# Performance work log

Hardware: AMD Instinct MI355X
Metric: run time of the kernel (lower is better)

The kernel has to match this reference:

```python
import jax, jax.numpy as jnp
import numpy as np

B, T, D, H = 32, 8192, 128, 128

def setup_inputs() -> dict:
    key = jax.random.key(0)
    k1, k2, k3, k4, k5 = jax.random.split(key, 5)
    return {
        "encoder_outputs": jax.random.normal(k1, (B, T, D), dtype=jnp.float32),
        "decoder_hidden": jax.random.normal(k2, (B, H), dtype=jnp.float32),
        "W1": jax.random.normal(k3, (D, D), dtype=jnp.float32) * 0.08,
        "W2": jax.random.normal(k4, (H, D), dtype=jnp.float32) * 0.08,
        "V": jax.random.normal(k5, (D, 1), dtype=jnp.float32) * 0.08,
    }

def reference(encoder_outputs, decoder_hidden, W1, W2, V):
    # score: [B, T, D] = tanh(enc @ W1 + (dec @ W2)[:, None, :])
    score = jnp.tanh(jnp.einsum('btd,de->bte', encoder_outputs, W1)
                     + jnp.einsum('bh,hd->bd', decoder_hidden, W2)[:, None, :])
    # logits: [B, T, 1]; softmax over time axis (axis=1)
    logits = jnp.einsum('btd,do->bto', score, V)
    attention_weights = jax.nn.softmax(logits, axis=1)
    # context: [B, D] weighted sum over T
    context_vector = jnp.sum(attention_weights * encoder_outputs, axis=1)
    return context_vector, attention_weights
```

## Files before the change

### kernel.cpp

```cpp
#include <hip/hip_runtime.h>

#define B_ 32
#define T_ 8192
#define D_ 128
#define MBLK 128
#define NCHUNK 64

typedef __attribute__((ext_vector_type(8))) _Float16 half8;
typedef __attribute__((ext_vector_type(4))) _Float16 half4;
typedef __attribute__((ext_vector_type(4))) float floatx4;

__device__ __forceinline__ float tanh_fast(float x) {
    float e = __expf(2.0f * x);
    return 1.0f - __fdividef(2.0f, e + 1.0f);
}

__global__ void prep_kernel(const float* __restrict__ W1, half8* __restrict__ W1frag,
                            const float* __restrict__ dec, const float* __restrict__ W2,
                            float* __restrict__ bias) {
    int bid = blockIdx.x, tid = threadIdx.x;
    if (bid < 8) {
        int tg = bid * 256 + tid;
        int kk = tg >> 9, ni = (tg >> 6) & 7, lane = tg & 63;
        half8 h;
        #pragma unroll
        for (int j = 0; j < 8; ++j) {
            int k = kk * 32 + ((lane >> 4) * 8) + j;
            int n = ni * 16 + (lane & 15);
            h[j] = (_Float16)W1[k * 128 + n];
        }
        W1frag[tg] = h;
    } else {
        int b = (bid - 8) * 2 + (tid >> 7);
        int d = tid & 127;
        float acc = 0.f;
        for (int h = 0; h < 128; ++h)
            acc += dec[b * 128 + h] * W2[h * 128 + d];
        bias[b * 128 + d] = acc;
    }
}

__global__ __launch_bounds__(512)
void main_kernel(const float* __restrict__ enc, const half8* __restrict__ W1frag,
                 const float* __restrict__ bias, const float* __restrict__ V,
                 float* __restrict__ out_w, float* __restrict__ s_part,
                 float* __restrict__ c_part)
{
    __shared__ __align__(16) char smem_u[32768];
    __shared__ __align__(16) float red[MBLK];
    __shared__ __align__(16) float ews[MBLK];
    __shared__ __align__(16) float c_red[8][128];
    __shared__ float sp[2];

    half8* bfr = (half8*)smem_u;
    char*  encl = smem_u;

    const int tid = threadIdx.x;
    const int l = tid & 63;
    const int w = tid >> 6;
    const int g = l >> 4;
    const int bid = blockIdx.x;
    const int b = bid >> 6;
    const int chunk = bid & 63;
    const int arow = w * 16 + (l & 15);
    const float* rowp = enc + ((long)b * T_ + (long)chunk * MBLK + arow) * D_ + g * 8;

    #pragma unroll
    for (int q = 0; q < 4; ++q)
        __builtin_amdgcn_global_load_lds(
            (const __attribute__((address_space(1))) void*)(W1frag + q * 512 + tid),
            (__attribute__((address_space(3))) void*)(bfr + q * 512 + (w << 6)),
            16, 0, 0);

    half8 afr[4];
    #pragma unroll
    for (int kk = 0; kk < 4; ++kk) {
        float4 f0 = *(const float4*)(rowp + kk * 32);
        float4 f1 = *(const float4*)(rowp + kk * 32 + 4);
        half8 a;
        a[0] = (_Float16)f0.x; a[1] = (_Float16)f0.y;
        a[2] = (_Float16)f0.z; a[3] = (_Float16)f0.w;
        a[4] = (_Float16)f1.x; a[5] = (_Float16)f1.y;
        a[6] = (_Float16)f1.z; a[7] = (_Float16)f1.w;
        afr[kk] = a;
    }

    float bs[8], vv[8];
    #pragma unroll
    for (int ni = 0; ni < 8; ++ni) {
        int n = ni * 16 + (l & 15);
        bs[ni] = bias[b * 128 + n];
        vv[ni] = V[n];
    }
    __syncthreads();

    floatx4 acc[8];
    #pragma unroll
    for (int ni = 0; ni < 8; ++ni) acc[ni] = (floatx4)0.0f;

    #pragma unroll
    for (int kk = 0; kk < 4; ++kk)
        #pragma unroll
        for (int ni = 0; ni < 8; ++ni)
            acc[ni] = __builtin_amdgcn_mfma_f32_16x16x32_f16(
                          afr[kk], bfr[(kk * 8 + ni) * 64 + l], acc[ni], 0, 0, 0);

    __syncthreads();

    {
        const int asw = (arow & 7) << 4;
        #pragma unroll
        for (int kk = 0; kk < 4; ++kk) {
            int byte = arow * 256 + (((kk * 64) + (g * 16)) ^ asw);
            *(half8*)(encl + byte) = afr[kk];
        }
    }

    float p[4];
    #pragma unroll
    for (int j2 = 0; j2 < 4; ++j2) {
        float q = 0.f;
        #pragma unroll
        for (int ni = 0; ni < 8; ++ni)
            q += tanh_fast(acc[ni][j2] + bs[ni]) * vv[ni];
        #pragma unroll
        for (int mk = 1; mk < 16; mk <<= 1)
            q += __shfl_xor(q, mk);
        p[j2] = q;
    }
    if ((l & 15) == 0) {
        floatx4 v4 = {p[0], p[1], p[2], p[3]};
        *(floatx4*)(&red[w * 16 + g * 4]) = v4;
        *(floatx4*)(out_w + (long)b * T_ + chunk * MBLK + w * 16 + g * 4) = v4;
    }
    __syncthreads();

    if (tid < 128) {
        float ew = __expf(red[tid]);
        ews[tid] = ew;
        float s = ew;
        #pragma unroll
        for (int mk = 1; mk < 64; mk <<= 1) s += __shfl_xor(s, mk);
        if ((tid & 63) == 0) sp[tid >> 6] = s;
    }
    __syncthreads();
    if (tid == 0) s_part[b * NCHUNK + chunk] = sp[0] + sp[1];

    if (tid < 256) {
        const int rg = tid >> 5, dg = tid & 31;
        floatx4 cc = (floatx4)0.0f;
        #pragma unroll
        for (int rr = 0; rr < 16; ++rr) {
            int r = rg * 16 + rr;
            float wgt = ews[r];
            half4 h = *(const half4*)(encl + (r * 256 + ((dg * 8) ^ ((r & 7) << 4))));
            #pragma unroll
            for (int i = 0; i < 4; ++i) cc[i] += wgt * (float)h[i];
        }
        *(floatx4*)(&c_red[rg][dg * 4]) = cc;
    }
    __syncthreads();
    if (tid < 128) {
        float s = 0.f;
        #pragma unroll
        for (int gg = 0; gg < 8; ++gg) s += c_red[gg][tid];
        c_part[((long)b * NCHUNK + chunk) * 128 + tid] = s;
    }
}

__global__ __launch_bounds__(256)
void tail_kernel(const float* __restrict__ s_part, const float* __restrict__ c_part,
                 float* __restrict__ ctx, float* __restrict__ out_w)
{
    __shared__ float stats[1];
    __shared__ float part[2][128];
    int bid = blockIdx.x, tid = threadIdx.x;
    int b = bid >> 4, j = bid & 15;

    if (tid < 64) {
        float s = s_part[b * 64 + tid];
        #pragma unroll
        for (int mk = 1; mk < 64; mk <<= 1) s += __shfl_xor(s, mk);
        if (tid == 0) stats[0] = __fdividef(1.0f, s);
    }
    __syncthreads();
    float inv = stats[0];

    if (j == 0) {
        int d = tid & 127, h = tid >> 7;
        float acc = 0.f;
        #pragma unroll 4
        for (int ch = h * 32; ch < h * 32 + 32; ++ch)
            acc += c_part[((long)b * 64 + ch) * 128 + d];
        part[h][d] = acc;
        __syncthreads();
        if (tid < 128)
            ctx[b * 128 + tid] = (part[0][tid] + part[1][tid]) * inv;
    }

    float* ow = out_w + (long)b * T_ + j * 512;
    #pragma unroll
    for (int q = 0; q < 2; ++q) {
        int i = q * 256 + tid;
        ow[i] = __expf(ow[i]) * inv;
    }
}

extern "C" void kernel_launch(void* const* d_in, const int* in_sizes, int n_in,
                              void* d_out, int out_size, void* d_ws, size_t ws_size,
                              hipStream_t stream)
{
    const float* enc = (const float*)d_in[0];
    const float* dec = (const float*)d_in[1];
    const float* W1  = (const float*)d_in[2];
    const float* W2  = (const float*)d_in[3];
    const float* V   = (const float*)d_in[4];

    float* ctx  = (float*)d_out;
    float* outw = ctx + B_ * D_;

    float* ws     = (float*)d_ws;
    float* bias   = ws;
    float* s_part = bias + 4096;
    float* c_part = s_part + 2048;
    half8* W1frag = (half8*)(c_part + (long)B_ * NCHUNK * 128);

    prep_kernel<<<24, 256, 0, stream>>>(W1, W1frag, dec, W2, bias);
    main_kernel<<<B_ * NCHUNK, 512, 0, stream>>>(enc, W1frag, bias, V, outw, s_part, c_part);
    tail_kernel<<<B_ * 16, 256, 0, stream>>>(s_part, c_part, ctx, outw);
}
```

Before: 49.61 us.

## Process two chunks per block with register prefetch of next encoder tile

Each block now handles two consecutive 128-row chunks. The W1 fragment LDS load is amortized over both chunks, and the next chunk's encoder rows are prefetched into registers while the current chunk runs its MFMA and softmax work. W1 fragments and the encoder staging buffer now get separate LDS regions instead of aliasing, which removes one barrier per chunk. The costs are more LDS per block, more live registers, and half as many blocks (1024), which may leave the GPU less full. Launch bounds now request 4 waves per EU.

```diff
diff --git a/kernel.cpp b/kernel.cpp
--- a/kernel.cpp
+++ b/kernel.cpp
@@ -5,6 +5,7 @@
 #define D_ 128
 #define MBLK 128
 #define NCHUNK 64
+#define CPB 2
 
 typedef __attribute__((ext_vector_type(8))) _Float16 half8;
 typedef __attribute__((ext_vector_type(4))) _Float16 half4;
@@ -40,50 +41,35 @@
     }
 }
 
-__global__ __launch_bounds__(512)
+__global__ __launch_bounds__(512, 4)
 void main_kernel(const float* __restrict__ enc, const half8* __restrict__ W1frag,
                  const float* __restrict__ bias, const float* __restrict__ V,
                  float* __restrict__ out_w, float* __restrict__ s_part,
                  float* __restrict__ c_part)
 {
-    __shared__ __align__(16) char smem_u[32768];
+    __shared__ __align__(16) half8 bfr[2048];
+    __shared__ __align__(16) char encl[32768];
     __shared__ __align__(16) float red[MBLK];
     __shared__ __align__(16) float ews[MBLK];
     __shared__ __align__(16) float c_red[8][128];
     __shared__ float sp[2];
-
-    half8* bfr = (half8*)smem_u;
-    char*  encl = smem_u;
 
     const int tid = threadIdx.x;
     const int l = tid & 63;
     const int w = tid >> 6;
     const int g = l >> 4;
     const int bid = blockIdx.x;
-    const int b = bid >> 6;
-    const int chunk = bid & 63;
+    const int b = bid >> 5;
+    const int cbase = (bid & 31) * CPB;
     const int arow = w * 16 + (l & 15);
-    const float* rowp = enc + ((long)b * T_ + (long)chunk * MBLK + arow) * D_ + g * 8;
-
-    #pragma unroll
-    for (int q = 0; q < 4; ++q)
+    const float* rowp = enc + ((long)b * T_ + (long)cbase * MBLK + arow) * D_ + g * 8;
+
+    #pragma unroll
+    for (int qi = 0; qi < 4; ++qi)
         __builtin_amdgcn_global_load_lds(
-            (const __attribute__((address_space(1))) void*)(W1frag + q * 512 + tid),
-            (__attribute__((address_space(3))) void*)(bfr + q * 512 + (w << 6)),
+            (const __attribute__((address_space(1))) void*)(W1frag + qi * 512 + tid),
+            (__attribute__((address_space(3))) void*)(bfr + qi * 512 + (w << 6)),
             16, 0, 0);
-
-    half8 afr[4];
-    #pragma unroll
-    for (int kk = 0; kk < 4; ++kk) {
-        float4 f0 = *(const float4*)(rowp + kk * 32);
-        float4 f1 = *(const float4*)(rowp + kk * 32 + 4);
-        half8 a;
-        a[0] = (_Float16)f0.x; a[1] = (_Float16)f0.y;
-        a[2] = (_Float16)f0.z; a[3] = (_Float16)f0.w;
-        a[4] = (_Float16)f1.x; a[5] = (_Float16)f1.y;
-        a[6] = (_Float16)f1.z; a[7] = (_Float16)f1.w;
-        afr[kk] = a;
-    }
 
     float bs[8], vv[8];
     #pragma unroll
@@ -92,79 +78,109 @@
         bs[ni] = bias[b * 128 + n];
         vv[ni] = V[n];
     }
+
+    float4 f0[4], f1[4];
+    #pragma unroll
+    for (int kk = 0; kk < 4; ++kk) {
+        f0[kk] = *(const float4*)(rowp + kk * 32);
+        f1[kk] = *(const float4*)(rowp + kk * 32 + 4);
+    }
     __syncthreads();
 
-    floatx4 acc[8];
-    #pragma unroll
-    for (int ni = 0; ni < 8; ++ni) acc[ni] = (floatx4)0.0f;
-
-    #pragma unroll
-    for (int kk = 0; kk < 4; ++kk)
-        #pragma unroll
-        for (int ni = 0; ni < 8; ++ni)
-            acc[ni] = __builtin_amdgcn_mfma_f32_16x16x32_f16(
-                          afr[kk], bfr[(kk * 8 + ni) * 64 + l], acc[ni], 0, 0, 0);
-
-    __syncthreads();
-
-    {
-        const int asw = (arow & 7) << 4;
+    #pragma unroll 1
+    for (int ci = 0; ci < CPB; ++ci) {
+        const int chunk = cbase + ci;
+
+        half8 afr[4];
         #pragma unroll
         for (int kk = 0; kk < 4; ++kk) {
-            int byte = arow * 256 + (((kk * 64) + (g * 16)) ^ asw);
-            *(half8*)(encl + byte) = afr[kk];
-        }
-    }
-
-    float p[4];
-    #pragma unroll
-    for (int j2 = 0; j2 < 4; ++j2) {
-        float q = 0.f;
-        #pragma unroll
-        for (int ni = 0; ni < 8; ++ni)
-            q += tanh_fast(acc[ni][j2] + bs[ni]) * vv[ni];
-        #pragma unroll
-        for (int mk = 1; mk < 16; mk <<= 1)
-            q += __shfl_xor(q, mk);
-        p[j2] = q;
-    }
-    if ((l & 15) == 0) {
-        floatx4 v4 = {p[0], p[1], p[2], p[3]};
-        *(floatx4*)(&red[w * 16 + g * 4]) = v4;
-        *(floatx4*)(out_w + (long)b * T_ + chunk * MBLK + w * 16 + g * 4) = v4;
-    }
-    __syncthreads();
-
-    if (tid < 128) {
-        float ew = __expf(red[tid]);
-        ews[tid] = ew;
-        float s = ew;
-        #pragma unroll
-        for (int mk = 1; mk < 64; mk <<= 1) s += __shfl_xor(s, mk);
-        if ((tid & 63) == 0) sp[tid >> 6] = s;
-    }
-    __syncthreads();
-    if (tid == 0) s_part[b * NCHUNK + chunk] = sp[0] + sp[1];
-
-    if (tid < 256) {
-        const int rg = tid >> 5, dg = tid & 31;
-        floatx4 cc = (floatx4)0.0f;
-        #pragma unroll
-        for (int rr = 0; rr < 16; ++rr) {
-            int r = rg * 16 + rr;
-            float wgt = ews[r];
-            half4 h = *(const half4*)(encl + (r * 256 + ((dg * 8) ^ ((r & 7) << 4))));
-            #pragma unroll
-            for (int i = 0; i < 4; ++i) cc[i] += wgt * (float)h[i];
-        }
-        *(floatx4*)(&c_red[rg][dg * 4]) = cc;
-    }
-    __syncthreads();
-    if (tid < 128) {
-        float s = 0.f;
-        #pragma unroll
-        for (int gg = 0; gg < 8; ++gg) s += c_red[gg][tid];
-        c_part[((long)b * NCHUNK + chunk) * 128 + tid] = s;
+            half8 a;
+            a[0] = (_Float16)f0[kk].x; a[1] = (_Float16)f0[kk].y;
+            a[2] = (_Float16)f0[kk].z; a[3] = (_Float16)f0[kk].w;
+            a[4] = (_Float16)f1[kk].x; a[5] = (_Float16)f1[kk].y;
+            a[6] = (_Float16)f1[kk].z; a[7] = (_Float16)f1[kk].w;
+            afr[kk] = a;
+        }
+
+        if (ci < CPB - 1) {
+            rowp += MBLK * D_;
+            #pragma unroll
+            for (int kk = 0; kk < 4; ++kk) {
+                f0[kk] = *(const float4*)(rowp + kk * 32);
+                f1[kk] = *(const float4*)(rowp + kk * 32 + 4);
+            }
+        }
+
+        {
+            const int asw = (arow & 7) << 4;
+            #pragma unroll
+            for (int kk = 0; kk < 4; ++kk) {
+                int byte = arow * 256 + (((kk * 64) + (g * 16)) ^ asw);
+                *(half8*)(encl + byte) = afr[kk];
+            }
+        }
+
+        floatx4 acc[8];
+        #pragma unroll
+        for (int ni = 0; ni < 8; ++ni) acc[ni] = (floatx4)0.0f;
+
+        #pragma unroll
+        for (int kk = 0; kk < 4; ++kk)
+            #pragma unroll
+            for (int ni = 0; ni < 8; ++ni)
+                acc[ni] = __builtin_amdgcn_mfma_f32_16x16x32_f16(
+                              afr[kk], bfr[(kk * 8 + ni) * 64 + l], acc[ni], 0, 0, 0);
+
+        float p[4];
+        #pragma unroll
+        for (int j2 = 0; j2 < 4; ++j2) {
+            float q = 0.f;
+            #pragma unroll
+            for (int ni = 0; ni < 8; ++ni)
+                q += tanh_fast(acc[ni][j2] + bs[ni]) * vv[ni];
+            #pragma unroll
+            for (int mk = 1; mk < 16; mk <<= 1)
+                q += __shfl_xor(q, mk);
+            p[j2] = q;
+        }
+        if ((l & 15) == 0) {
+            floatx4 v4 = {p[0], p[1], p[2], p[3]};
+            *(floatx4*)(&red[w * 16 + g * 4]) = v4;
+            *(floatx4*)(out_w + (long)b * T_ + chunk * MBLK + w * 16 + g * 4) = v4;
+        }
+        __syncthreads();
+
+        if (tid < 128) {
+            float ew = __expf(red[tid]);
+            ews[tid] = ew;
+            float s = ew;
+            #pragma unroll
+            for (int mk = 1; mk < 64; mk <<= 1) s += __shfl_xor(s, mk);
+            if ((tid & 63) == 0) sp[tid >> 6] = s;
+        }
+        __syncthreads();
+        if (tid == 0) s_part[b * NCHUNK + chunk] = sp[0] + sp[1];
+
+        if (tid < 256) {
+            const int rg = tid >> 5, dg = tid & 31;
+            floatx4 cc = (floatx4)0.0f;
+            #pragma unroll
+            for (int rr = 0; rr < 16; ++rr) {
+                int r = rg * 16 + rr;
+                float wgt = ews[r];
+                half4 h = *(const half4*)(encl + (r * 256 + ((dg * 8) ^ ((r & 7) << 4))));
+                #pragma unroll
+                for (int i = 0; i < 4; ++i) cc[i] += wgt * (float)h[i];
+            }
+            *(floatx4*)(&c_red[rg][dg * 4]) = cc;
+        }
+        __syncthreads();
+        if (tid < 128) {
+            float s = 0.f;
+            #pragma unroll
+            for (int gg = 0; gg < 8; ++gg) s += c_red[gg][tid];
+            c_part[((long)b * NCHUNK + chunk) * 128 + tid] = s;
+        }
     }
 }
 
@@ -226,6 +242,6 @@
     half8* W1frag = (half8*)(c_part + (long)B_ * NCHUNK * 128);
 
     prep_kernel<<<24, 256, 0, stream>>>(W1, W1frag, dec, W2, bias);
-    main_kernel<<<B_ * NCHUNK, 512, 0, stream>>>(enc, W1frag, bias, V, outw, s_part, c_part);
+    main_kernel<<<B_ * (NCHUNK / CPB), 512, 0, stream>>>(enc, W1frag, bias, V, outw, s_part, c_part);
     tail_kernel<<<B_ * 16, 256, 0, stream>>>(s_part, c_part, ctx, outw);
 }
```

After: 69.72 us. +40.5%, slower.
